# Kernel tuning notes

Hardware: AMD Instinct MI355X
Metric: run time of the kernel (lower is better)

Reference implementation:

```python
import jax, jax.numpy as jnp
import numpy as np

NV, NH = 6000, 6000
DV, DH = 1024, 1024
HID, HEADS = 128, 3
EV, EH, EC = 200000, 200000, 32768


def _gat(x, ei, W, a_src, a_dst, bias, edge_attr=None, lin_e=None, a_e=None):
    """PyG GATConv (heads=H, concat=False, add_self_loops=True, LeakyReLU 0.2).
    Returns (node_out [N,C], alpha [E+N, H])."""
    N = x.shape[0]
    H, C = a_src.shape
    xw = (x @ W).reshape(N, H, C)                      # [N,H,C]
    asrc = jnp.einsum('nhc,hc->nh', xw, a_src)         # [N,H]
    adst = jnp.einsum('nhc,hc->nh', xw, a_dst)
    loop = jnp.arange(N, dtype=ei.dtype)               # self-loops appended
    src = jnp.concatenate([ei[0], loop])
    dst = jnp.concatenate([ei[1], loop])
    alpha = asrc[src] + adst[dst]                      # [E+N,H]
    if edge_attr is not None:
        # edge_dim=1 path: lin_edge(weight)[E,H,C] dotted with att_edge; self-loop attr = mean (PyG fill_value='mean')
        ea = jnp.concatenate([edge_attr, jnp.full((N,), jnp.mean(edge_attr), edge_attr.dtype)])
        ef = (ea[:, None] * lin_e[None, :]).reshape(-1, H, C)
        alpha = alpha + jnp.einsum('ehc,hc->eh', ef, a_e)
    alpha = jax.nn.leaky_relu(alpha, 0.2)
    # segment softmax over incoming edges of each destination node
    amax = jax.ops.segment_max(alpha, dst, num_segments=N)
    ex = jnp.exp(alpha - amax[dst])
    den = jax.ops.segment_sum(ex, dst, num_segments=N)
    alpha = ex / (den[dst] + 1e-16)
    out = jax.ops.segment_sum(xw[src] * alpha[..., None], dst, num_segments=N)
    return out.mean(axis=1) + bias, alpha              # concat=False -> head mean


def _bn(x, g, b):  # BatchNorm1d, training mode (batch stats, biased var)
    m = x.mean(0)
    v = x.var(0)
    return (x - m) / jnp.sqrt(v + 1e-5) * g + b


def reference(virus_data, host_data, coexistence_data, virus_edge_weight, host_edge_weight,
              vW, v_asrc, v_adst, v_bias, v_line, v_atte,
              hW, h_asrc, h_adst, h_bias, h_line, h_atte,
              vhW, vh_asrc, vh_adst, vh_bias,
              hvW, hv_asrc, hv_adst, hv_bias,
              linv_W, linv_b, linh_W, linh_b, bn_g, bn_b,
              virus_edge_index, host_edge_index, coexistence_edge_index, coexistence_edge_index_t):
    feat_v, alpha_v = _gat(virus_data, virus_edge_index, vW, v_asrc, v_adst, v_bias,
                           virus_edge_weight, v_line, v_atte)
    feat_h, alpha_h = _gat(host_data, host_edge_index, hW, h_asrc, h_adst, h_bias,
                           host_edge_weight, h_line, h_atte)
    feat_vh, alpha_vh = _gat(coexistence_data, coexistence_edge_index_t, vhW, vh_asrc, vh_adst, vh_bias)
    feat_hv, alpha_hv = _gat(coexistence_data.T, coexistence_edge_index, hvW, hv_asrc, hv_adst, hv_bias)

    vh = jax.nn.leaky_relu(_bn(virus_data @ linv_W + linv_b, bn_g, bn_b), 0.01)
    hh = jax.nn.leaky_relu(_bn(host_data @ linh_W + linh_b, bn_g, bn_b), 0.01)

    output_host = vh @ hh.T                  # [Nv,Nh]
    output_virus = (hh @ vh.T).T             # [Nv,Nh]
    return (output_host, output_virus, output_host + output_virus,
            alpha_v, alpha_h, alpha_vh, alpha_hv,
            feat_v, feat_h, feat_vh, feat_hv)


def setup_inputs() -> dict:
    key = jax.random.key(0)
    ks = iter(jax.random.split(key, 48))

    def nrm(shape, s=0.05):
        return (jax.random.normal(next(ks), shape, jnp.float32) * s).astype(jnp.float32)

    def gat_params(din, edge=True):
        p = [nrm((din, HEADS * HID)), nrm((HEADS, HID)), nrm((HEADS, HID)), jnp.zeros((HID,), jnp.float32)]
        if edge:
            p += [nrm((HEADS * HID,)), nrm((HEADS, HID))]
        return p

    inp = {
        'virus_data': jax.random.normal(next(ks), (NV, DV), jnp.float32),
        'host_data': jax.random.normal(next(ks), (NH, DH), jnp.float32),
        'coexistence_data': jax.random.normal(next(ks), (DV, DH), jnp.float32),
        'virus_edge_weight': jax.random.uniform(next(ks), (EV,), jnp.float32),
        'host_edge_weight': jax.random.uniform(next(ks), (EH,), jnp.float32),
    }
    for pref, din, edge in [('v', DV, True), ('h', DH, True)]:
        W, asrc, adst, b, le, ae = gat_params(din, True)
        inp.update({f'{pref}W': W, f'{pref}_asrc': asrc, f'{pref}_adst': adst,
                    f'{pref}_bias': b, f'{pref}_line': le, f'{pref}_atte': ae})
    for pref, din in [('vh', DH), ('hv', DV)]:
        W, asrc, adst, b = gat_params(din, False)
        inp.update({f'{pref}W': W, f'{pref}_asrc': asrc, f'{pref}_adst': adst, f'{pref}_bias': b})
    inp.update({
        'linv_W': nrm((DV, HID)), 'linv_b': jnp.zeros((HID,), jnp.float32),
        'linh_W': nrm((DH, HID)), 'linh_b': jnp.zeros((HID,), jnp.float32),
        'bn_g': jnp.ones((HID,), jnp.float32), 'bn_b': jnp.zeros((HID,), jnp.float32),
        'virus_edge_index': jax.random.randint(next(ks), (2, EV), 0, NV, jnp.int32),
        'host_edge_index': jax.random.randint(next(ks), (2, EH), 0, NH, jnp.int32),
        'coexistence_edge_index': jax.random.randint(next(ks), (2, EC), 0, DH, jnp.int32),
        'coexistence_edge_index_t': jax.random.randint(next(ks), (2, EC), 0, DV, jnp.int32),
    })
    return inp
```

## Files before the change

kernel.cpp:

```cpp
#include <hip/hip_runtime.h>

#define NV   6000
#define NH   6000
#define HID  128
#define EV   200000
#define EH   200000
#define EC   32768

typedef __attribute__((ext_vector_type(8))) short bf16x8;
typedef __attribute__((ext_vector_type(4))) float f32x4;

__device__ __forceinline__ unsigned short f2bf(float f){
  unsigned u = __float_as_uint(f);
  u += 0x7FFFu + ((u >> 16) & 1u);
  return (unsigned short)(u >> 16);
}

__global__ __launch_bounds__(256) void k_prep_cv(
    const float* __restrict__ virus, const float* __restrict__ hostd, const float* __restrict__ coex,
    unsigned short* __restrict__ Avb, unsigned short* __restrict__ Ahb, unsigned short* __restrict__ Acb){
  int i = blockIdx.x * 256 + threadIdx.x;
  const float* src; unsigned short* dst; int off;
  if (i < 1536000)      { src = virus; dst = Avb; off = i; }
  else if (i < 3072000) { src = hostd; dst = Ahb; off = i - 1536000; }
  else                  { src = coex;  dst = Acb; off = i - 3072000; }
  float4 v = reinterpret_cast<const float4*>(src)[off];
  ushort4 o; o.x = f2bf(v.x); o.y = f2bf(v.y); o.z = f2bf(v.z); o.w = f2bf(v.w);
  reinterpret_cast<ushort4*>(dst)[off] = o;
}

__global__ __launch_bounds__(256) void k_prep_tp(
    const float* __restrict__ coex, const float* __restrict__ vW, const float* __restrict__ linvW,
    const float* __restrict__ hW, const float* __restrict__ linhW,
    const float* __restrict__ vhW, const float* __restrict__ hvW,
    unsigned short* __restrict__ Actb, unsigned short* __restrict__ BtV,
    unsigned short* __restrict__ BtH, unsigned short* __restrict__ BtVH,
    unsigned short* __restrict__ BtHV){
  int idx = blockIdx.x * 256 + threadIdx.x;
  const float* src; unsigned short* dst; int Nc, off, local;
  if      (idx < 1048576){ src=coex;  dst=Actb; Nc=1024; off=0;   local=idx; }
  else if (idx < 1441792){ src=vW;    dst=BtV;  Nc=384;  off=0;   local=idx-1048576; }
  else if (idx < 1572864){ src=linvW; dst=BtV;  Nc=128;  off=384; local=idx-1441792; }
  else if (idx < 1966080){ src=hW;    dst=BtH;  Nc=384;  off=0;   local=idx-1572864; }
  else if (idx < 2097152){ src=linhW; dst=BtH;  Nc=128;  off=384; local=idx-1966080; }
  else if (idx < 2490368){ src=vhW;   dst=BtVH; Nc=384;  off=0;   local=idx-2097152; }
  else                   { src=hvW;   dst=BtHV; Nc=384;  off=0;   local=idx-2490368; }
  int n = local >> 10, k = local & 1023;
  dst[(size_t)(n + off) * 1024 + k] = f2bf(src[(size_t)k * Nc + n]);
}

template<bool TRIPLE>
__device__ __forceinline__ void gemm_nt_body(
    const unsigned short* __restrict__ A, const unsigned short* __restrict__ B,
    int M, int N, int K, int lda, int ldb,
    float* __restrict__ C0, float* __restrict__ C1o, float* __restrict__ C2o, int ldc,
    int bx, int by)
{
  const int tid  = threadIdx.x;
  const int lane = tid & 63, w = tid >> 6;
  const int wr = w >> 1, wc = w & 1;
  const int R  = by * 128 + wr * 64;
  const int Cb = bx * 128 + wc * 64;
  const int r0 = lane & 15, kg = lane >> 4;

  const unsigned short* pa[4]; const unsigned short* pb[4];
  bool va[4], vb[4];
#pragma unroll
  for (int i = 0; i < 4; i++){
    int row = R + i * 16 + r0;
    va[i] = row < M;
    pa[i] = A + (size_t)(va[i] ? row : 0) * lda + kg * 8;
    int col = Cb + i * 16 + r0;
    vb[i] = col < N;
    pb[i] = B + (size_t)(vb[i] ? col : 0) * ldb + kg * 8;
  }
  const bf16x8 Z8 = {0,0,0,0,0,0,0,0};
  f32x4 acc[4][4];
#pragma unroll
  for (int i = 0; i < 4; i++)
#pragma unroll
    for (int j = 0; j < 4; j++) acc[i][j] = (f32x4){0.f,0.f,0.f,0.f};

  for (int kk = 0; kk < K; kk += 32){
    bf16x8 av[4], bv[4];
#pragma unroll
    for (int i = 0; i < 4; i++){
      bf16x8 ta = *reinterpret_cast<const bf16x8*>(pa[i] + kk);
      bf16x8 tb = *reinterpret_cast<const bf16x8*>(pb[i] + kk);
      av[i] = va[i] ? ta : Z8;
      bv[i] = vb[i] ? tb : Z8;
    }
#pragma unroll
    for (int i = 0; i < 4; i++)
#pragma unroll
      for (int j = 0; j < 4; j++)
        acc[i][j] = __builtin_amdgcn_mfma_f32_16x16x32_bf16(av[i], bv[j], acc[i][j], 0, 0, 0);
  }

  const int cn = lane & 15, rq = (lane >> 4) * 4;
#pragma unroll
  for (int i = 0; i < 4; i++){
    int row0 = R + i * 16 + rq;
#pragma unroll
    for (int j = 0; j < 4; j++){
      int col = Cb + j * 16 + cn;
      if (col < N){
#pragma unroll
        for (int r = 0; r < 4; r++){
          int row = row0 + r;
          if (row < M){
            size_t idx = (size_t)row * ldc + col;
            float v = acc[i][j][r];
            C0[idx] = v;
            if (TRIPLE){ C1o[idx] = v; C2o[idx] = v + v; }
          }
        }
      }
    }
  }
}

__global__ __launch_bounds__(256) void k_gemm4(
    const unsigned short* A0, const unsigned short* B0, float* Co0,
    const unsigned short* A1, const unsigned short* B1, float* Co1,
    const unsigned short* A2, const unsigned short* B2, float* Co2,
    const unsigned short* A3, const unsigned short* B3, float* Co3)
{
  int z = blockIdx.z;
  if (z == 0)
    gemm_nt_body<false>(A0, B0, NV, 512, 1024, 1024, 1024, Co0, nullptr, nullptr, 512, blockIdx.x, blockIdx.y);
  else if (z == 1)
    gemm_nt_body<false>(A1, B1, NH, 512, 1024, 1024, 1024, Co1, nullptr, nullptr, 512, blockIdx.x, blockIdx.y);
  else {
    if (blockIdx.x >= 3 || blockIdx.y >= 8) return;
    if (z == 2)
      gemm_nt_body<false>(A2, B2, 1024, 384, 1024, 1024, 1024, Co2, nullptr, nullptr, 384, blockIdx.x, blockIdx.y);
    else
      gemm_nt_body<false>(A3, B3, 1024, 384, 1024, 1024, 1024, Co3, nullptr, nullptr, 384, blockIdx.x, blockIdx.y);
  }
}

__global__ __launch_bounds__(256) void k_gemm_final(
    const unsigned short* __restrict__ A, const unsigned short* __restrict__ B,
    float* __restrict__ o0, float* __restrict__ o1, float* __restrict__ o2)
{
  gemm_nt_body<true>(A, B, NV, NH, 128, 128, 128, o0, o1, o2, NH, blockIdx.x, blockIdx.y);
}

__global__ __launch_bounds__(128) void k_scal(
    const float* vW, const float* v_as, const float* v_ad,
    const float* hW, const float* h_as, const float* h_ad,
    const float* vhW, const float* vh_as, const float* vh_ad,
    const float* hvW, const float* hv_as, const float* hv_ad,
    float* WasV, float* WadV, float* WasH, float* WadH,
    float* WasC1, float* WadC1, float* WasC2, float* WadC2,
    const float* vew, const float* hew, float* sums,
    const float* v_line, const float* v_atte, const float* h_line, const float* h_atte,
    float* Kbuf)
{
  int b = blockIdx.x, t = threadIdx.x;
  int lane = t & 63, w = t >> 6;
  __shared__ float sh[2][2];
  if (b < 4096){
    const float *W, *as_, *ad_; float *Was, *Wad;
    switch (b >> 10){
      case 0:  W=vW;  as_=v_as;  ad_=v_ad;  Was=WasV;  Wad=WadV;  break;
      case 1:  W=hW;  as_=h_as;  ad_=h_ad;  Was=WasH;  Wad=WadH;  break;
      case 2:  W=vhW; as_=vh_as; ad_=vh_ad; Was=WasC1; Wad=WadC1; break;
      default: W=hvW; as_=hv_as; ad_=hv_ad; Was=WasC2; Wad=WadC2; break;
    }
    int k = b & 1023;
    const float* Wr = W + (size_t)k * 384;
    for (int h = 0; h < 3; h++){
      float x = Wr[h*128 + t];
      float s = x * as_[h*128 + t], d = x * ad_[h*128 + t];
      for (int off = 32; off > 0; off >>= 1){ s += __shfl_down(s, off); d += __shfl_down(d, off); }
      if (lane == 0){ sh[w][0] = s; sh[w][1] = d; }
      __syncthreads();
      if (t == 0){ Was[k*3+h] = sh[0][0] + sh[1][0]; Wad[k*3+h] = sh[0][1] + sh[1][1]; }
      __syncthreads();
    }
  } else if (b < 4352){
    const float* x = (b < 4224) ? vew : hew;
    int slot = (b < 4224) ? 0 : 1;
    int base = (b - 4096) & 127;
    float s = 0.f;
    for (int i = base*128 + t; i < EV; i += 128*128) s += x[i];
    for (int off = 32; off > 0; off >>= 1) s += __shfl_down(s, off);
    if (lane == 0) sh[w][0] = s;
    __syncthreads();
    if (t == 0) atomicAdd(&sums[slot], sh[0][0] + sh[1][0]);
  } else {
    for (int h = 0; h < 3; h++){
      float s = v_line[h*128+t] * v_atte[h*128+t];
      for (int off = 32; off > 0; off >>= 1) s += __shfl_down(s, off);
      if (lane == 0) sh[w][0] = s;
      __syncthreads();
      if (t == 0) Kbuf[h] = sh[0][0] + sh[1][0];
      __syncthreads();
      s = h_line[h*128+t] * h_atte[h*128+t];
      for (int off = 32; off > 0; off >>= 1) s += __shfl_down(s, off);
      if (lane == 0) sh[w][0] = s;
      __syncthreads();
      if (t == 0) Kbuf[3+h] = sh[0][0] + sh[1][0];
      __syncthreads();
    }
  }
}

__global__ __launch_bounds__(256) void k_nodedot(
    const float* __restrict__ virus, const float* __restrict__ hostd, const float* __restrict__ coex,
    const float* __restrict__ WasV, const float* __restrict__ WadV,
    const float* __restrict__ WasH, const float* __restrict__ WadH,
    const float* __restrict__ WasC1, const float* __restrict__ WadC1,
    float* asV, float* adV, float* asH, float* adH, float* asC1, float* adC1)
{
  int b = blockIdx.x, t = threadIdx.x;
  const float *xb, *Was, *Wad; float *ao, *doo;
  if (b < 6000)       { int n=b;        xb=virus+(size_t)n*1024; Was=WasV;  Wad=WadV;  ao=asV+n*3;  doo=adV+n*3; }
  else if (b < 12000) { int n=b-6000;   xb=hostd+(size_t)n*1024; Was=WasH;  Wad=WadH;  ao=asH+n*3;  doo=adH+n*3; }
  else                { int n=b-12000;  xb=coex +(size_t)n*1024; Was=WasC1; Wad=WadC1; ao=asC1+n*3; doo=adC1+n*3; }
  float v[6] = {0,0,0,0,0,0};
  for (int k = t; k < 1024; k += 256){
    float xv = xb[k];
    v[0] += xv * Was[k*3+0]; v[1] += xv * Was[k*3+1]; v[2] += xv * Was[k*3+2];
    v[3] += xv * Wad[k*3+0]; v[4] += xv * Wad[k*3+1]; v[5] += xv * Wad[k*3+2];
  }
  __shared__ float sh[4][6];
  int lane = t & 63, w = t >> 6;
  for (int off = 32; off > 0; off >>= 1)
#pragma unroll
    for (int i = 0; i < 6; i++) v[i] += __shfl_down(v[i], off);
  if (lane == 0)
#pragma unroll
    for (int i = 0; i < 6; i++) sh[w][i] = v[i];
  __syncthreads();
  if (t < 6){
    float r = sh[0][t] + sh[1][t] + sh[2][t] + sh[3][t];
    if (t < 3) ao[t] = r; else doo[t-3] = r;
  }
}

__global__ __launch_bounds__(256) void k_nodedot_t(
    const float* __restrict__ coex, const float* __restrict__ Was, const float* __restrict__ Wad,
    float* __restrict__ as_, float* __restrict__ ad_)
{
  __shared__ float sw[3072], sd[3072];
  for (int i = threadIdx.x; i < 3072; i += 256){ sw[i] = Was[i]; sd[i] = Wad[i]; }
  __syncthreads();
  int nn = blockIdx.x * 256 + threadIdx.x;
  float a0=0,a1=0,a2=0,b0=0,b1=0,b2=0;
  for (int k = 0; k < 1024; k++){
    float xv = coex[(size_t)k*1024 + nn];
    a0 += xv*sw[k*3];   a1 += xv*sw[k*3+1]; a2 += xv*sw[k*3+2];
    b0 += xv*sd[k*3];   b1 += xv*sd[k*3+1]; b2 += xv*sd[k*3+2];
  }
  as_[nn*3]=a0; as_[nn*3+1]=a1; as_[nn*3+2]=a2;
  ad_[nn*3]=b0; ad_[nn*3+1]=b1; ad_[nn*3+2]=b2;
}

__global__ __launch_bounds__(256) void k_hist4(
    const int* vd, const int* hd, const int* c1d, const int* c2d,
    int* cV, int* cH, int* c1, int* c2)
{
  int idx = blockIdx.x * 256 + threadIdx.x;
  if (idx >= EV + EH + 2*EC) return;
  const int* dp; int* cnt; int e;
  if      (idx < EV)          { dp=vd;  cnt=cV; e=idx; }
  else if (idx < EV+EH)       { dp=hd;  cnt=cH; e=idx-EV; }
  else if (idx < EV+EH+EC)    { dp=c1d; cnt=c1; e=idx-EV-EH; }
  else                        { dp=c2d; cnt=c2; e=idx-EV-EH-EC; }
  atomicAdd(&cnt[dp[e]], 1);
}

__global__ __launch_bounds__(256) void k_exscan4(
    int* cV, int* sV, int* cH, int* sH, int* c1, int* s1, int* c2, int* s2)
{
  int* cnt; int* st; int N;
  switch (blockIdx.x){
    case 0:  cnt=cV; st=sV; N=NV;   break;
    case 1:  cnt=cH; st=sH; N=NH;   break;
    case 2:  cnt=c1; st=s1; N=1024; break;
    default: cnt=c2; st=s2; N=1024; break;
  }
  __shared__ int sh[256];
  int t = threadIdx.x;
  int chunk = (N + 255) >> 8;
  int lo = t * chunk, hi = lo + chunk;
  if (hi > N) hi = N;
  if (lo > N) lo = N;
  int s = 0;
  for (int i = lo; i < hi; i++) s += cnt[i];
  sh[t] = s;
  __syncthreads();
  for (int off = 1; off < 256; off <<= 1){
    int v = (t >= off) ? sh[t - off] : 0;
    __syncthreads();
    sh[t] += v;
    __syncthreads();
  }
  int run = sh[t] - s;
  for (int i = lo; i < hi; i++){ st[i] = run; run += cnt[i]; }
  if (t == 255) st[N] = sh[255];
}

__global__ __launch_bounds__(256) void k_scatter4(
    const int* vd, const int* hd, const int* c1d, const int* c2d,
    const int* stV, const int* stH, const int* st1, const int* st2,
    int* cuV, int* cuH, int* cu1, int* cu2,
    int* soV, int* soH, int* so1, int* so2)
{
  int idx = blockIdx.x * 256 + threadIdx.x;
  if (idx >= EV + EH + 2*EC) return;
  const int* dp; const int* st; int* cur; int* so; int e;
  if      (idx < EV)       { dp=vd;  st=stV; cur=cuV; so=soV; e=idx; }
  else if (idx < EV+EH)    { dp=hd;  st=stH; cur=cuH; so=soH; e=idx-EV; }
  else if (idx < EV+EH+EC) { dp=c1d; st=st1; cur=cu1; so=so1; e=idx-EV-EH; }
  else                     { dp=c2d; st=st2; cur=cu2; so=so2; e=idx-EV-EH-EC; }
  int d = dp[e];
  so[st[d] + atomicAdd(&cur[d], 1)] = e;
}

#define GCAP 512
struct GatDesc {
  const float* xw; const int* src; const int* sorted; const int* starts;
  const float* as_; const float* ad_; const float* Kc; const float* ew; const float* sumw;
  const float* bias; float* alpha; float* feat;
  int ld; int E; float invE;
};

__global__ __launch_bounds__(128) void k_gat(GatDesc d){
  const int n = blockIdx.x, t = threadIdx.x;
  const int lane = t & 63, w = t >> 6;
  __shared__ float shx[GCAP][3];
  __shared__ int   shs[GCAP];
  __shared__ float redA[2][3], redB[2][3];
  const int s0 = d.starts[n];
  const int deg = d.starts[n+1] - s0;
  const bool hasW = (d.ew != nullptr);
  float K0=0.f, K1=0.f, K2=0.f, wself=0.f;
  if (hasW){ K0=d.Kc[0]; K1=d.Kc[1]; K2=d.Kc[2]; wself = d.sumw[0] * d.invE; }
  const float ad0 = d.ad_[n*3], ad1 = d.ad_[n*3+1], ad2 = d.ad_[n*3+2];
  float sr0 = d.as_[n*3+0] + ad0 + wself*K0;  sr0 = sr0 >= 0.f ? sr0 : 0.2f*sr0;
  float sr1 = d.as_[n*3+1] + ad1 + wself*K1;  sr1 = sr1 >= 0.f ? sr1 : 0.2f*sr1;
  float sr2 = d.as_[n*3+2] + ad2 + wself*K2;  sr2 = sr2 >= 0.f ? sr2 : 0.2f*sr2;

  float mx0 = sr0, mx1 = sr1, mx2 = sr2;
  for (int i = t; i < deg; i += 128){
    int e = d.sorted[s0 + i];
    int s = d.src[e];
    float wv = hasW ? d.ew[e] : 0.f;
    float r0 = d.as_[s*3+0] + ad0 + wv*K0;  r0 = r0 >= 0.f ? r0 : 0.2f*r0;
    float r1 = d.as_[s*3+1] + ad1 + wv*K1;  r1 = r1 >= 0.f ? r1 : 0.2f*r1;
    float r2 = d.as_[s*3+2] + ad2 + wv*K2;  r2 = r2 >= 0.f ? r2 : 0.2f*r2;
    if (i < GCAP){ shs[i] = s; shx[i][0]=r0; shx[i][1]=r1; shx[i][2]=r2; }
    mx0 = fmaxf(mx0, r0); mx1 = fmaxf(mx1, r1); mx2 = fmaxf(mx2, r2);
  }
  for (int off = 32; off > 0; off >>= 1){
    mx0 = fmaxf(mx0, __shfl_down(mx0, off));
    mx1 = fmaxf(mx1, __shfl_down(mx1, off));
    mx2 = fmaxf(mx2, __shfl_down(mx2, off));
  }
  if (lane == 0){ redA[w][0]=mx0; redA[w][1]=mx1; redA[w][2]=mx2; }
  __syncthreads();
  const float M0 = fmaxf(redA[0][0], redA[1][0]);
  const float M1 = fmaxf(redA[0][1], redA[1][1]);
  const float M2 = fmaxf(redA[0][2], redA[1][2]);

  float t0 = 0.f, t1 = 0.f, t2 = 0.f;
  for (int i = t; i < deg; i += 128){
    float r0, r1, r2;
    if (i < GCAP){ r0 = shx[i][0]; r1 = shx[i][1]; r2 = shx[i][2]; }
    else {
      int e = d.sorted[s0 + i]; int s = d.src[e];
      float wv = hasW ? d.ew[e] : 0.f;
      r0 = d.as_[s*3+0] + ad0 + wv*K0; r0 = r0>=0.f?r0:0.2f*r0;
      r1 = d.as_[s*3+1] + ad1 + wv*K1; r1 = r1>=0.f?r1:0.2f*r1;
      r2 = d.as_[s*3+2] + ad2 + wv*K2; r2 = r2>=0.f?r2:0.2f*r2;
    }
    float e0 = expf(r0 - M0), e1 = expf(r1 - M1), e2 = expf(r2 - M2);
    if (i < GCAP){ shx[i][0]=e0; shx[i][1]=e1; shx[i][2]=e2; }
    t0 += e0; t1 += e1; t2 += e2;
  }
  for (int off = 32; off > 0; off >>= 1){
    t0 += __shfl_down(t0, off); t1 += __shfl_down(t1, off); t2 += __shfl_down(t2, off);
  }
  if (lane == 0){ redB[w][0]=t0; redB[w][1]=t1; redB[w][2]=t2; }
  __syncthreads();
  const float se0 = expf(sr0 - M0), se1 = expf(sr1 - M1), se2 = expf(sr2 - M2);
  const float i0 = 1.f / (redB[0][0] + redB[1][0] + se0 + 1e-16f);
  const float i1 = 1.f / (redB[0][1] + redB[1][1] + se1 + 1e-16f);
  const float i2 = 1.f / (redB[0][2] + redB[1][2] + se2 + 1e-16f);

  for (int i = t; i < deg; i += 128){
    int e = d.sorted[s0 + i];
    float e0, e1, e2;
    if (i < GCAP){ e0 = shx[i][0]; e1 = shx[i][1]; e2 = shx[i][2]; }
    else {
      int s = d.src[e];
      float wv = hasW ? d.ew[e] : 0.f;
      float r0 = d.as_[s*3+0]+ad0+wv*K0; r0=r0>=0.f?r0:0.2f*r0;
      float r1 = d.as_[s*3+1]+ad1+wv*K1; r1=r1>=0.f?r1:0.2f*r1;
      float r2 = d.as_[s*3+2]+ad2+wv*K2; r2=r2>=0.f?r2:0.2f*r2;
      e0 = expf(r0-M0); e1 = expf(r1-M1); e2 = expf(r2-M2);
    }
    float* ap = d.alpha + (size_t)e * 3;
    ap[0] = e0 * i0; ap[1] = e1 * i1; ap[2] = e2 * i2;
  }
  if (t == 0){
    float* ap = d.alpha + (size_t)(d.E + n) * 3;
    ap[0] = se0 * i0; ap[1] = se1 * i1; ap[2] = se2 * i2;
  }

  const float* xn = d.xw + (size_t)n * d.ld;
  float f0 = xn[t] * se0, f1 = xn[128+t] * se1, f2 = xn[256+t] * se2;
  for (int i = 0; i < deg; i++){
    int s; float e0, e1, e2;
    if (i < GCAP){ s = shs[i]; e0 = shx[i][0]; e1 = shx[i][1]; e2 = shx[i][2]; }
    else {
      int e = d.sorted[s0 + i]; s = d.src[e];
      float wv = hasW ? d.ew[e] : 0.f;
      float r0 = d.as_[s*3+0]+ad0+wv*K0; r0=r0>=0.f?r0:0.2f*r0;
      float r1 = d.as_[s*3+1]+ad1+wv*K1; r1=r1>=0.f?r1:0.2f*r1;
      float r2 = d.as_[s*3+2]+ad2+wv*K2; r2=r2>=0.f?r2:0.2f*r2;
      e0 = expf(r0-M0); e1 = expf(r1-M1); e2 = expf(r2-M2);
    }
    const float* xs = d.xw + (size_t)s * d.ld;
    f0 += xs[t] * e0; f1 += xs[128+t] * e1; f2 += xs[256+t] * e2;
  }
  d.feat[(size_t)n*128 + t] = (f0*i0 + f1*i1 + f2*i2) * (1.f/3.f) + d.bias[t];
}

__global__ __launch_bounds__(128) void k_bnstat(
    const float* __restrict__ C1, const float* __restrict__ C2, float* __restrict__ bnacc)
{
  int which = blockIdx.y, t = threadIdx.x;
  const float* C = which ? C2 : C1;
  int r0 = blockIdx.x * 32;
  float s = 0.f, q = 0.f;
  for (int r = 0; r < 32; r++){
    int row = r0 + r;
    if (row < NV){
      float v = C[(size_t)row * 512 + 384 + t];
      s += v; q += v * v;
    }
  }
  atomicAdd(&bnacc[which*256 + t],       s);
  atomicAdd(&bnacc[which*256 + 128 + t], q);
}

__global__ __launch_bounds__(256) void k_bnfin(
    const float* __restrict__ bnacc, float* meanV, float* rstdV, float* meanH, float* rstdH)
{
  int t = threadIdx.x;
  int which = t >> 7, j = t & 127;
  float mu = bnacc[which*256 + j] * (1.f/NV);
  float var = bnacc[which*256 + 128 + j] * (1.f/NV) - mu*mu;
  if (which == 0){ meanV[j] = mu; rstdV[j] = rsqrtf(var + 1e-5f); }
  else           { meanH[j] = mu; rstdH[j] = rsqrtf(var + 1e-5f); }
}

__global__ __launch_bounds__(256) void k_bnapply(
    const float* __restrict__ C1, const float* __restrict__ C2,
    const float* __restrict__ meanV, const float* __restrict__ rstdV,
    const float* __restrict__ meanH, const float* __restrict__ rstdH,
    const float* __restrict__ g, const float* __restrict__ b,
    unsigned short* __restrict__ vhb, unsigned short* __restrict__ hhb)
{
  int idx = blockIdx.x * 256 + threadIdx.x;
  int which = idx >= 768000;
  int local = which ? idx - 768000 : idx;
  int m = local >> 7, j = local & 127;
  const float* C = which ? C2 : C1;
  const float* mean = which ? meanH : meanV;
  const float* rstd = which ? rstdH : rstdV;
  unsigned short* out = which ? hhb : vhb;
  float v = (C[(size_t)m*512 + 384 + j] - mean[j]) * rstd[j] * g[j] + b[j];
  v = v >= 0.f ? v : 0.01f * v;
  out[local] = f2bf(v);
}

extern "C" void kernel_launch(void* const* d_in, const int* in_sizes, int n_in,
                              void* d_out, int out_size, void* d_ws, size_t ws_size,
                              hipStream_t stream)
{
  (void)in_sizes; (void)n_in; (void)out_size; (void)ws_size;
  const float* virus  = (const float*)d_in[0];
  const float* hostd  = (const float*)d_in[1];
  const float* coex   = (const float*)d_in[2];
  const float* vew    = (const float*)d_in[3];
  const float* hew    = (const float*)d_in[4];
  const float* vW     = (const float*)d_in[5];
  const float* v_as   = (const float*)d_in[6];
  const float* v_ad   = (const float*)d_in[7];
  const float* v_bias = (const float*)d_in[8];
  const float* v_line = (const float*)d_in[9];
  const float* v_atte = (const float*)d_in[10];
  const float* hW     = (const float*)d_in[11];
  const float* h_as   = (const float*)d_in[12];
  const float* h_ad   = (const float*)d_in[13];
  const float* h_bias = (const float*)d_in[14];
  const float* h_line = (const float*)d_in[15];
  const float* h_atte = (const float*)d_in[16];
  const float* vhW    = (const float*)d_in[17];
  const float* vh_as  = (const float*)d_in[18];
  const float* vh_ad  = (const float*)d_in[19];
  const float* vh_bias= (const float*)d_in[20];
  const float* hvW    = (const float*)d_in[21];
  const float* hv_as  = (const float*)d_in[22];
  const float* hv_ad  = (const float*)d_in[23];
  const float* hv_bias= (const float*)d_in[24];
  const float* linvW  = (const float*)d_in[25];
  const float* linhW  = (const float*)d_in[27];
  const float* bng    = (const float*)d_in[29];
  const float* bnb    = (const float*)d_in[30];
  const int* vei  = (const int*)d_in[31];
  const int* hei  = (const int*)d_in[32];
  const int* cei  = (const int*)d_in[33];
  const int* ceit = (const int*)d_in[34];

  float* out = (float*)d_out;
  float* o0 = out;
  float* o1 = out + 36000000ll;
  float* o2 = out + 72000000ll;
  float* alpha_v  = out + 108000000ll;
  float* alpha_h  = alpha_v  + 618000;
  float* alpha_vh = alpha_h  + 618000;
  float* alpha_hv = alpha_vh + 101376;
  float* feat_v   = alpha_hv + 101376;
  float* feat_h   = feat_v   + 768000;
  float* feat_vh  = feat_h   + 768000;
  float* feat_hv  = feat_vh  + 131072;

  char* wp = (char*)d_ws;
  auto alloc = [&](size_t b) -> void* { void* p = wp; wp += (b + 255) & ~(size_t)255; return p; };
  float* C1 = (float*)alloc((size_t)NV*512*4);
  float* C2 = (float*)alloc((size_t)NH*512*4);
  float* C3 = (float*)alloc((size_t)1024*384*4);
  float* C4 = (float*)alloc((size_t)1024*384*4);
  unsigned short* Avb  = (unsigned short*)alloc((size_t)NV*1024*2);
  unsigned short* Ahb  = (unsigned short*)alloc((size_t)NH*1024*2);
  unsigned short* Acb  = (unsigned short*)alloc((size_t)1024*1024*2);
  unsigned short* Actb = (unsigned short*)alloc((size_t)1024*1024*2);
  unsigned short* BtV  = (unsigned short*)alloc((size_t)512*1024*2);
  unsigned short* BtH  = (unsigned short*)alloc((size_t)512*1024*2);
  unsigned short* BtVH = (unsigned short*)alloc((size_t)384*1024*2);
  unsigned short* BtHV = (unsigned short*)alloc((size_t)384*1024*2);
  unsigned short* vhb  = (unsigned short*)alloc((size_t)NV*128*2);
  unsigned short* hhb  = (unsigned short*)alloc((size_t)NH*128*2);
  float* asV  = (float*)alloc(NV*3*4);   float* adV  = (float*)alloc(NV*3*4);
  float* asH  = (float*)alloc(NH*3*4);   float* adH  = (float*)alloc(NH*3*4);
  float* asC1 = (float*)alloc(1024*3*4); float* adC1 = (float*)alloc(1024*3*4);
  float* asC2 = (float*)alloc(1024*3*4); float* adC2 = (float*)alloc(1024*3*4);
  float* WasV = (float*)alloc(1024*3*4); float* WadV = (float*)alloc(1024*3*4);
  float* WasH = (float*)alloc(1024*3*4); float* WadH = (float*)alloc(1024*3*4);
  float* WasC1= (float*)alloc(1024*3*4); float* WadC1= (float*)alloc(1024*3*4);
  float* WasC2= (float*)alloc(1024*3*4); float* WadC2= (float*)alloc(1024*3*4);
  int* startsV  = (int*)alloc((NV+1)*4);  int* sortedV  = (int*)alloc((size_t)EV*4);
  int* startsH  = (int*)alloc((NH+1)*4);  int* sortedH  = (int*)alloc((size_t)EH*4);
  int* startsC1 = (int*)alloc(1025*4);    int* sortedC1 = (int*)alloc((size_t)EC*4);
  int* startsC2 = (int*)alloc(1025*4);    int* sortedC2 = (int*)alloc((size_t)EC*4);
  float* meanV = (float*)alloc(512); float* rstdV = (float*)alloc(512);
  float* meanH = (float*)alloc(512); float* rstdH = (float*)alloc(512);
  float* Kbuf  = (float*)alloc(256);
  char* z0 = wp;
  int* cntV  = (int*)alloc(NV*4);   int* curV  = (int*)alloc(NV*4);
  int* cntH  = (int*)alloc(NH*4);   int* curH  = (int*)alloc(NH*4);
  int* cntC1 = (int*)alloc(1024*4); int* curC1 = (int*)alloc(1024*4);
  int* cntC2 = (int*)alloc(1024*4); int* curC2 = (int*)alloc(1024*4);
  float* sums  = (float*)alloc(256);
  float* bnacc = (float*)alloc(2*256*4);
  hipMemsetAsync(z0, 0, (size_t)(wp - z0), stream);

  const int* vsrc = vei,  *vdst = vei  + EV;
  const int* hsrc = hei,  *hdst = hei  + EH;
  const int* c1src= ceit, *c1dst= ceit + EC;
  const int* c2src= cei,  *c2dst= cei  + EC;

  k_prep_cv<<<13024, 256, 0, stream>>>(virus, hostd, coex, Avb, Ahb, Acb);
  k_prep_tp<<<11264, 256, 0, stream>>>(coex, vW, linvW, hW, linhW, vhW, hvW,
                                       Actb, BtV, BtH, BtVH, BtHV);
  k_gemm4<<<dim3(4,47,4), 256, 0, stream>>>(Avb, BtV, C1, Ahb, BtH, C2,
                                            Acb, BtVH, C3, Actb, BtHV, C4);
  k_scal<<<4353, 128, 0, stream>>>(vW, v_as, v_ad, hW, h_as, h_ad,
                                   vhW, vh_as, vh_ad, hvW, hv_as, hv_ad,
                                   WasV, WadV, WasH, WadH, WasC1, WadC1, WasC2, WadC2,
                                   vew, hew, sums, v_line, v_atte, h_line, h_atte, Kbuf);
  k_nodedot<<<13024, 256, 0, stream>>>(virus, hostd, coex,
                                       WasV, WadV, WasH, WadH, WasC1, WadC1,
                                       asV, adV, asH, adH, asC1, adC1);
  k_nodedot_t<<<4, 256, 0, stream>>>(coex, WasC2, WadC2, asC2, adC2);
  k_hist4<<<1819, 256, 0, stream>>>(vdst, hdst, c1dst, c2dst, cntV, cntH, cntC1, cntC2);
  k_exscan4<<<4, 256, 0, stream>>>(cntV, startsV, cntH, startsH, cntC1, startsC1, cntC2, startsC2);
  k_scatter4<<<1819, 256, 0, stream>>>(vdst, hdst, c1dst, c2dst,
                                       startsV, startsH, startsC1, startsC2,
                                       curV, curH, curC1, curC2,
                                       sortedV, sortedH, sortedC1, sortedC2);
  {
    GatDesc dv = { C1, vsrc, sortedV, startsV, asV, adV, Kbuf,   vew, &sums[0], v_bias,
                   alpha_v, feat_v, 512, EV, 1.f/EV };
    GatDesc dh = { C2, hsrc, sortedH, startsH, asH, adH, Kbuf+3, hew, &sums[1], h_bias,
                   alpha_h, feat_h, 512, EH, 1.f/EH };
    GatDesc d1 = { C3, c1src, sortedC1, startsC1, asC1, adC1, nullptr, nullptr, nullptr, vh_bias,
                   alpha_vh, feat_vh, 384, EC, 0.f };
    GatDesc d2 = { C4, c2src, sortedC2, startsC2, asC2, adC2, nullptr, nullptr, nullptr, hv_bias,
                   alpha_hv, feat_hv, 384, EC, 0.f };
    k_gat<<<NV,   128, 0, stream>>>(dv);
    k_gat<<<NH,   128, 0, stream>>>(dh);
    k_gat<<<1024, 128, 0, stream>>>(d1);
    k_gat<<<1024, 128, 0, stream>>>(d2);
  }
  k_bnstat<<<dim3(188,2), 128, 0, stream>>>(C1, C2, bnacc);
  k_bnfin<<<1, 256, 0, stream>>>(bnacc, meanV, rstdV, meanH, rstdH);
  k_bnapply<<<6000, 256, 0, stream>>>(C1, C2, meanV, rstdV, meanH, rstdH, bng, bnb, vhb, hhb);
  k_gemm_final<<<dim3(47,47), 256, 0, stream>>>(vhb, hhb, o0, o1, o2);
}
```

Measured before the change: 957.2 us.

## Fuse prep, scalar, histogram, scan, GEMM and GAT stages into fewer kernels

The launch sequence collapses into five kernels. Prep, weight transpose, attention-weight folding, edge histogram and edge-weight sums now share one launch. Scan and node dots share another, the GEMMs share a launch with the CSR scatter, and the four GAT layers are merged with the BatchNorm statistics. The final GEMM applies BatchNorm and leaky-ReLU on the fly, and GEMM outputs are stored as bf16. The transpose now goes through LDS tiles. Together these cut launch count, intermediate fp32 traffic and the separate BN passes, at the cost of bf16 rounding of the xw features and more complex kernels.

```diff
diff --git a/kernel.cpp b/kernel.cpp
--- a/kernel.cpp
+++ b/kernel.cpp
@@ -2,10 +2,10 @@
 
 #define NV   6000
 #define NH   6000
-#define HID  128
 #define EV   200000
 #define EH   200000
 #define EC   32768
+#define GCAP 256
 
 typedef __attribute__((ext_vector_type(8))) short bf16x8;
 typedef __attribute__((ext_vector_type(4))) float f32x4;
@@ -15,45 +15,232 @@
   u += 0x7FFFu + ((u >> 16) & 1u);
   return (unsigned short)(u >> 16);
 }
-
-__global__ __launch_bounds__(256) void k_prep_cv(
+__device__ __forceinline__ float bf2f(unsigned short h){
+  return __uint_as_float((unsigned)h << 16);
+}
+
+__global__ __launch_bounds__(256) void k_prep(
     const float* __restrict__ virus, const float* __restrict__ hostd, const float* __restrict__ coex,
-    unsigned short* __restrict__ Avb, unsigned short* __restrict__ Ahb, unsigned short* __restrict__ Acb){
-  int i = blockIdx.x * 256 + threadIdx.x;
-  const float* src; unsigned short* dst; int off;
-  if (i < 1536000)      { src = virus; dst = Avb; off = i; }
-  else if (i < 3072000) { src = hostd; dst = Ahb; off = i - 1536000; }
-  else                  { src = coex;  dst = Acb; off = i - 3072000; }
-  float4 v = reinterpret_cast<const float4*>(src)[off];
-  ushort4 o; o.x = f2bf(v.x); o.y = f2bf(v.y); o.z = f2bf(v.z); o.w = f2bf(v.w);
-  reinterpret_cast<ushort4*>(dst)[off] = o;
-}
-
-__global__ __launch_bounds__(256) void k_prep_tp(
-    const float* __restrict__ coex, const float* __restrict__ vW, const float* __restrict__ linvW,
+    const float* __restrict__ vW, const float* __restrict__ linvW,
     const float* __restrict__ hW, const float* __restrict__ linhW,
     const float* __restrict__ vhW, const float* __restrict__ hvW,
-    unsigned short* __restrict__ Actb, unsigned short* __restrict__ BtV,
-    unsigned short* __restrict__ BtH, unsigned short* __restrict__ BtVH,
-    unsigned short* __restrict__ BtHV){
-  int idx = blockIdx.x * 256 + threadIdx.x;
-  const float* src; unsigned short* dst; int Nc, off, local;
-  if      (idx < 1048576){ src=coex;  dst=Actb; Nc=1024; off=0;   local=idx; }
-  else if (idx < 1441792){ src=vW;    dst=BtV;  Nc=384;  off=0;   local=idx-1048576; }
-  else if (idx < 1572864){ src=linvW; dst=BtV;  Nc=128;  off=384; local=idx-1441792; }
-  else if (idx < 1966080){ src=hW;    dst=BtH;  Nc=384;  off=0;   local=idx-1572864; }
-  else if (idx < 2097152){ src=linhW; dst=BtH;  Nc=128;  off=384; local=idx-1966080; }
-  else if (idx < 2490368){ src=vhW;   dst=BtVH; Nc=384;  off=0;   local=idx-2097152; }
-  else                   { src=hvW;   dst=BtHV; Nc=384;  off=0;   local=idx-2490368; }
-  int n = local >> 10, k = local & 1023;
-  dst[(size_t)(n + off) * 1024 + k] = f2bf(src[(size_t)k * Nc + n]);
-}
-
-template<bool TRIPLE>
-__device__ __forceinline__ void gemm_nt_body(
+    const float* __restrict__ v_as, const float* __restrict__ v_ad,
+    const float* __restrict__ h_as, const float* __restrict__ h_ad,
+    const float* __restrict__ vh_as, const float* __restrict__ vh_ad,
+    const float* __restrict__ hv_as, const float* __restrict__ hv_ad,
+    const float* __restrict__ vew, const float* __restrict__ hew,
+    const float* __restrict__ v_line, const float* __restrict__ v_atte,
+    const float* __restrict__ h_line, const float* __restrict__ h_atte,
+    const int* __restrict__ vdst, const int* __restrict__ hdst,
+    const int* __restrict__ c1dst, const int* __restrict__ c2dst,
+    unsigned short* Avb, unsigned short* Ahb, unsigned short* Acb,
+    unsigned short* Actb, unsigned short* BtV, unsigned short* BtH,
+    unsigned short* BtVH, unsigned short* BtHV,
+    float* WasV, float* WadV, float* WasH, float* WadH,
+    float* WasC1, float* WadC1, float* WasC2, float* WadC2,
+    float* sums, float* Kbuf,
+    int* cntV, int* cntH, int* cntC1, int* cntC2)
+{
+  __shared__ float tp_lds[64][65];
+  __shared__ float red4[4][2];
+  int b = blockIdx.x, t = threadIdx.x;
+  int lane = t & 63, w = t >> 6;
+
+  if (b < 13024){
+    int i = b * 256 + t;
+    const float* src; unsigned short* dst; int off;
+    if (i < 1536000)      { src = virus; dst = Avb; off = i; }
+    else if (i < 3072000) { src = hostd; dst = Ahb; off = i - 1536000; }
+    else                  { src = coex;  dst = Acb; off = i - 3072000; }
+    float4 v = reinterpret_cast<const float4*>(src)[off];
+    ushort4 o; o.x = f2bf(v.x); o.y = f2bf(v.y); o.z = f2bf(v.z); o.w = f2bf(v.w);
+    reinterpret_cast<ushort4*>(dst)[off] = o;
+    return;
+  }
+  b -= 13024;
+  if (b < 704){
+    const float* src; unsigned short* dst; int Nc, roff, ntn, rel;
+    if      (b < 256){ src=coex;  dst=Actb; Nc=1024; roff=0;   ntn=16; rel=b; }
+    else if (b < 352){ src=vW;    dst=BtV;  Nc=384;  roff=0;   ntn=6;  rel=b-256; }
+    else if (b < 384){ src=linvW; dst=BtV;  Nc=128;  roff=384; ntn=2;  rel=b-352; }
+    else if (b < 480){ src=hW;    dst=BtH;  Nc=384;  roff=0;   ntn=6;  rel=b-384; }
+    else if (b < 512){ src=linhW; dst=BtH;  Nc=128;  roff=384; ntn=2;  rel=b-480; }
+    else if (b < 608){ src=vhW;   dst=BtVH; Nc=384;  roff=0;   ntn=6;  rel=b-512; }
+    else             { src=hvW;   dst=BtHV; Nc=384;  roff=0;   ntn=6;  rel=b-608; }
+    int tn = rel % ntn, tk = rel / ntn;
+    int k0 = tk * 64, n0 = tn * 64;
+    int tx = t & 63, ty = t >> 6;
+#pragma unroll
+    for (int r = 0; r < 16; r++)
+      tp_lds[ty + r*4][tx] = src[(size_t)(k0 + ty + r*4) * Nc + n0 + tx];
+    __syncthreads();
+#pragma unroll
+    for (int r = 0; r < 16; r++)
+      dst[(size_t)(n0 + ty + r*4 + roff) * 1024 + k0 + tx] = f2bf(tp_lds[tx][ty + r*4]);
+    return;
+  }
+  b -= 704;
+  if (b < 2048){
+    int m = b >> 9;
+    int krow = (b & 511) * 2 + (t >> 7);
+    int c = t & 127;
+    const float *W, *as_, *ad_; float *Was, *Wad;
+    switch (m){
+      case 0:  W=vW;  as_=v_as;  ad_=v_ad;  Was=WasV;  Wad=WadV;  break;
+      case 1:  W=hW;  as_=h_as;  ad_=h_ad;  Was=WasH;  Wad=WadH;  break;
+      case 2:  W=vhW; as_=vh_as; ad_=vh_ad; Was=WasC1; Wad=WadC1; break;
+      default: W=hvW; as_=hv_as; ad_=hv_ad; Was=WasC2; Wad=WadC2; break;
+    }
+    const float* Wr = W + (size_t)krow * 384;
+    for (int h = 0; h < 3; h++){
+      float x = Wr[h*128 + c];
+      float s = x * as_[h*128 + c], d = x * ad_[h*128 + c];
+      for (int off = 32; off > 0; off >>= 1){ s += __shfl_down(s, off); d += __shfl_down(d, off); }
+      if (lane == 0){ red4[w][0] = s; red4[w][1] = d; }
+      __syncthreads();
+      if (t == 0)  { Was[krow*3+h] = red4[0][0] + red4[1][0]; Wad[krow*3+h] = red4[0][1] + red4[1][1]; }
+      if (t == 128){ Was[krow*3+h] = red4[2][0] + red4[3][0]; Wad[krow*3+h] = red4[2][1] + red4[3][1]; }
+      __syncthreads();
+    }
+    return;
+  }
+  b -= 2048;
+  if (b < 1819){
+    int idx = b * 256 + t;
+    if (idx >= EV + EH + 2*EC) return;
+    const int* dp; int* cnt; int e;
+    if      (idx < EV)       { dp=vdst;  cnt=cntV;  e=idx; }
+    else if (idx < EV+EH)    { dp=hdst;  cnt=cntH;  e=idx-EV; }
+    else if (idx < EV+EH+EC) { dp=c1dst; cnt=cntC1; e=idx-EV-EH; }
+    else                     { dp=c2dst; cnt=cntC2; e=idx-EV-EH-EC; }
+    atomicAdd(&cnt[dp[e]], 1);
+    return;
+  }
+  b -= 1819;
+  if (b < 256){
+    int which = b >> 7, base = b & 127;
+    const float* x = which ? hew : vew;
+    float s = 0.f;
+    for (int i = base*256 + t; i < EV; i += 128*256) s += x[i];
+    for (int off = 32; off > 0; off >>= 1) s += __shfl_down(s, off);
+    if (lane == 0) red4[w][0] = s;
+    __syncthreads();
+    if (t == 0) atomicAdd(&sums[which], red4[0][0]+red4[1][0]+red4[2][0]+red4[3][0]);
+    return;
+  }
+  for (int h = 0; h < 3; h++){
+    float s = (t < 128) ? v_line[h*128+t] * v_atte[h*128+t] : 0.f;
+    for (int off = 32; off > 0; off >>= 1) s += __shfl_down(s, off);
+    if (lane == 0) red4[w][0] = s;
+    __syncthreads();
+    if (t == 0) Kbuf[h] = red4[0][0]+red4[1][0]+red4[2][0]+red4[3][0];
+    __syncthreads();
+    s = (t < 128) ? h_line[h*128+t] * h_atte[h*128+t] : 0.f;
+    for (int off = 32; off > 0; off >>= 1) s += __shfl_down(s, off);
+    if (lane == 0) red4[w][0] = s;
+    __syncthreads();
+    if (t == 0) Kbuf[3+h] = red4[0][0]+red4[1][0]+red4[2][0]+red4[3][0];
+    __syncthreads();
+  }
+}
+
+__global__ __launch_bounds__(256) void k_nd(
+    int* cntV, int* startsV, int* cntH, int* startsH,
+    int* cntC1, int* startsC1, int* cntC2, int* startsC2,
+    const float* __restrict__ virus, const float* __restrict__ hostd, const float* __restrict__ coex,
+    const float* __restrict__ WasV, const float* __restrict__ WadV,
+    const float* __restrict__ WasH, const float* __restrict__ WadH,
+    const float* __restrict__ WasC1, const float* __restrict__ WadC1,
+    const float* __restrict__ WasC2, const float* __restrict__ WadC2,
+    float* asV, float* adV, float* asH, float* adH,
+    float* asC1, float* adC1, float* asC2, float* adC2)
+{
+  __shared__ int   ssc[256];
+  __shared__ float sh6[4][6];
+  __shared__ float st[8][32][6];
+  int b = blockIdx.x, t = threadIdx.x;
+
+  if (b < 4){
+    int* cnt; int* st_; int N;
+    switch (b){
+      case 0:  cnt=cntV;  st_=startsV;  N=NV;   break;
+      case 1:  cnt=cntH;  st_=startsH;  N=NH;   break;
+      case 2:  cnt=cntC1; st_=startsC1; N=1024; break;
+      default: cnt=cntC2; st_=startsC2; N=1024; break;
+    }
+    int chunk = (N + 255) >> 8;
+    int lo = t * chunk, hi = lo + chunk;
+    if (hi > N) hi = N;
+    if (lo > N) lo = N;
+    int s = 0;
+    for (int i = lo; i < hi; i++) s += cnt[i];
+    ssc[t] = s;
+    __syncthreads();
+    for (int off = 1; off < 256; off <<= 1){
+      int v = (t >= off) ? ssc[t - off] : 0;
+      __syncthreads();
+      ssc[t] += v;
+      __syncthreads();
+    }
+    int run = ssc[t] - s;
+    for (int i = lo; i < hi; i++){ st_[i] = run; run += cnt[i]; }
+    if (t == 255) st_[N] = ssc[255];
+    return;
+  }
+  b -= 4;
+  if (b < 13024){
+    const float *xb, *Was, *Wad; float *ao, *doo;
+    if (b < 6000)       { xb=virus+(size_t)b*1024;        Was=WasV;  Wad=WadV;  ao=asV+b*3;          doo=adV+b*3; }
+    else if (b < 12000) { int n=b-6000;  xb=hostd+(size_t)n*1024; Was=WasH;  Wad=WadH;  ao=asH+n*3;  doo=adH+n*3; }
+    else                { int n=b-12000; xb=coex +(size_t)n*1024; Was=WasC1; Wad=WadC1; ao=asC1+n*3; doo=adC1+n*3; }
+    float v[6] = {0,0,0,0,0,0};
+    for (int k = t; k < 1024; k += 256){
+      float xv = xb[k];
+      v[0] += xv*Was[k*3+0]; v[1] += xv*Was[k*3+1]; v[2] += xv*Was[k*3+2];
+      v[3] += xv*Wad[k*3+0]; v[4] += xv*Wad[k*3+1]; v[5] += xv*Wad[k*3+2];
+    }
+    int lane = t & 63, w = t >> 6;
+    for (int off = 32; off > 0; off >>= 1)
+#pragma unroll
+      for (int i = 0; i < 6; i++) v[i] += __shfl_down(v[i], off);
+    if (lane == 0)
+#pragma unroll
+      for (int i = 0; i < 6; i++) sh6[w][i] = v[i];
+    __syncthreads();
+    if (t < 6){
+      float r = sh6[0][t] + sh6[1][t] + sh6[2][t] + sh6[3][t];
+      if (t < 3) ao[t] = r; else doo[t-3] = r;
+    }
+    return;
+  }
+  b -= 13024;
+  int c = t & 31, ks = t >> 5;
+  int nn = b * 32 + c;
+  float a[6] = {0,0,0,0,0,0};
+  for (int k = ks*128; k < ks*128 + 128; k++){
+    float xv = coex[(size_t)k*1024 + nn];
+    a[0] += xv*WasC2[k*3+0]; a[1] += xv*WasC2[k*3+1]; a[2] += xv*WasC2[k*3+2];
+    a[3] += xv*WadC2[k*3+0]; a[4] += xv*WadC2[k*3+1]; a[5] += xv*WadC2[k*3+2];
+  }
+#pragma unroll
+  for (int j = 0; j < 6; j++) st[ks][c][j] = a[j];
+  __syncthreads();
+  if (t < 32){
+    float r[6] = {0,0,0,0,0,0};
+#pragma unroll
+    for (int k = 0; k < 8; k++)
+#pragma unroll
+      for (int j = 0; j < 6; j++) r[j] += st[k][t][j];
+    int n2 = b * 32 + t;
+    asC2[n2*3] = r[0]; asC2[n2*3+1] = r[1]; asC2[n2*3+2] = r[2];
+    adC2[n2*3] = r[3]; adC2[n2*3+1] = r[4]; adC2[n2*3+2] = r[5];
+  }
+}
+
+template<int MODE>
+__device__ __forceinline__ void gemm_body(
     const unsigned short* __restrict__ A, const unsigned short* __restrict__ B,
-    int M, int N, int K, int lda, int ldb,
-    float* __restrict__ C0, float* __restrict__ C1o, float* __restrict__ C2o, int ldc,
+    int M, int N, unsigned short* __restrict__ xwb, float* __restrict__ lin,
     int bx, int by)
 {
   const int tid  = threadIdx.x;
@@ -69,10 +256,10 @@
   for (int i = 0; i < 4; i++){
     int row = R + i * 16 + r0;
     va[i] = row < M;
-    pa[i] = A + (size_t)(va[i] ? row : 0) * lda + kg * 8;
+    pa[i] = A + (size_t)(va[i] ? row : 0) * 1024 + kg * 8;
     int col = Cb + i * 16 + r0;
     vb[i] = col < N;
-    pb[i] = B + (size_t)(vb[i] ? col : 0) * ldb + kg * 8;
+    pb[i] = B + (size_t)(vb[i] ? col : 0) * 1024 + kg * 8;
   }
   const bf16x8 Z8 = {0,0,0,0,0,0,0,0};
   f32x4 acc[4][4];
@@ -81,7 +268,7 @@
 #pragma unroll
     for (int j = 0; j < 4; j++) acc[i][j] = (f32x4){0.f,0.f,0.f,0.f};
 
-  for (int kk = 0; kk < K; kk += 32){
+  for (int kk = 0; kk < 1024; kk += 32){
     bf16x8 av[4], bv[4];
 #pragma unroll
     for (int i = 0; i < 4; i++){
@@ -109,10 +296,13 @@
         for (int r = 0; r < 4; r++){
           int row = row0 + r;
           if (row < M){
-            size_t idx = (size_t)row * ldc + col;
             float v = acc[i][j][r];
-            C0[idx] = v;
-            if (TRIPLE){ C1o[idx] = v; C2o[idx] = v + v; }
+            if (MODE == 0){
+              if (col < 384) xwb[(size_t)row * 384 + col] = f2bf(v);
+              else           lin[(size_t)row * 128 + col - 384] = v;
+            } else {
+              xwb[(size_t)row * 384 + col] = f2bf(v);
+            }
           }
         }
       }
@@ -120,222 +310,79 @@
   }
 }
 
-__global__ __launch_bounds__(256) void k_gemm4(
-    const unsigned short* A0, const unsigned short* B0, float* Co0,
-    const unsigned short* A1, const unsigned short* B1, float* Co1,
-    const unsigned short* A2, const unsigned short* B2, float* Co2,
-    const unsigned short* A3, const unsigned short* B3, float* Co3)
-{
-  int z = blockIdx.z;
-  if (z == 0)
-    gemm_nt_body<false>(A0, B0, NV, 512, 1024, 1024, 1024, Co0, nullptr, nullptr, 512, blockIdx.x, blockIdx.y);
-  else if (z == 1)
-    gemm_nt_body<false>(A1, B1, NH, 512, 1024, 1024, 1024, Co1, nullptr, nullptr, 512, blockIdx.x, blockIdx.y);
-  else {
-    if (blockIdx.x >= 3 || blockIdx.y >= 8) return;
-    if (z == 2)
-      gemm_nt_body<false>(A2, B2, 1024, 384, 1024, 1024, 1024, Co2, nullptr, nullptr, 384, blockIdx.x, blockIdx.y);
-    else
-      gemm_nt_body<false>(A3, B3, 1024, 384, 1024, 1024, 1024, Co3, nullptr, nullptr, 384, blockIdx.x, blockIdx.y);
-  }
-}
-
-__global__ __launch_bounds__(256) void k_gemm_final(
-    const unsigned short* __restrict__ A, const unsigned short* __restrict__ B,
-    float* __restrict__ o0, float* __restrict__ o1, float* __restrict__ o2)
-{
-  gemm_nt_body<true>(A, B, NV, NH, 128, 128, 128, o0, o1, o2, NH, blockIdx.x, blockIdx.y);
-}
-
-__global__ __launch_bounds__(128) void k_scal(
-    const float* vW, const float* v_as, const float* v_ad,
-    const float* hW, const float* h_as, const float* h_ad,
-    const float* vhW, const float* vh_as, const float* vh_ad,
-    const float* hvW, const float* hv_as, const float* hv_ad,
-    float* WasV, float* WadV, float* WasH, float* WadH,
-    float* WasC1, float* WadC1, float* WasC2, float* WadC2,
-    const float* vew, const float* hew, float* sums,
-    const float* v_line, const float* v_atte, const float* h_line, const float* h_atte,
-    float* Kbuf)
-{
-  int b = blockIdx.x, t = threadIdx.x;
-  int lane = t & 63, w = t >> 6;
-  __shared__ float sh[2][2];
-  if (b < 4096){
-    const float *W, *as_, *ad_; float *Was, *Wad;
-    switch (b >> 10){
-      case 0:  W=vW;  as_=v_as;  ad_=v_ad;  Was=WasV;  Wad=WadV;  break;
-      case 1:  W=hW;  as_=h_as;  ad_=h_ad;  Was=WasH;  Wad=WadH;  break;
-      case 2:  W=vhW; as_=vh_as; ad_=vh_ad; Was=WasC1; Wad=WadC1; break;
-      default: W=hvW; as_=hv_as; ad_=hv_ad; Was=WasC2; Wad=WadC2; break;
-    }
-    int k = b & 1023;
-    const float* Wr = W + (size_t)k * 384;
-    for (int h = 0; h < 3; h++){
-      float x = Wr[h*128 + t];
-      float s = x * as_[h*128 + t], d = x * ad_[h*128 + t];
-      for (int off = 32; off > 0; off >>= 1){ s += __shfl_down(s, off); d += __shfl_down(d, off); }
-      if (lane == 0){ sh[w][0] = s; sh[w][1] = d; }
-      __syncthreads();
-      if (t == 0){ Was[k*3+h] = sh[0][0] + sh[1][0]; Wad[k*3+h] = sh[0][1] + sh[1][1]; }
-      __syncthreads();
-    }
-  } else if (b < 4352){
-    const float* x = (b < 4224) ? vew : hew;
-    int slot = (b < 4224) ? 0 : 1;
-    int base = (b - 4096) & 127;
-    float s = 0.f;
-    for (int i = base*128 + t; i < EV; i += 128*128) s += x[i];
-    for (int off = 32; off > 0; off >>= 1) s += __shfl_down(s, off);
-    if (lane == 0) sh[w][0] = s;
-    __syncthreads();
-    if (t == 0) atomicAdd(&sums[slot], sh[0][0] + sh[1][0]);
-  } else {
-    for (int h = 0; h < 3; h++){
-      float s = v_line[h*128+t] * v_atte[h*128+t];
-      for (int off = 32; off > 0; off >>= 1) s += __shfl_down(s, off);
-      if (lane == 0) sh[w][0] = s;
-      __syncthreads();
-      if (t == 0) Kbuf[h] = sh[0][0] + sh[1][0];
-      __syncthreads();
-      s = h_line[h*128+t] * h_atte[h*128+t];
-      for (int off = 32; off > 0; off >>= 1) s += __shfl_down(s, off);
-      if (lane == 0) sh[w][0] = s;
-      __syncthreads();
-      if (t == 0) Kbuf[3+h] = sh[0][0] + sh[1][0];
-      __syncthreads();
-    }
-  }
-}
-
-__global__ __launch_bounds__(256) void k_nodedot(
-    const float* __restrict__ virus, const float* __restrict__ hostd, const float* __restrict__ coex,
-    const float* __restrict__ WasV, const float* __restrict__ WadV,
-    const float* __restrict__ WasH, const float* __restrict__ WadH,
-    const float* __restrict__ WasC1, const float* __restrict__ WadC1,
-    float* asV, float* adV, float* asH, float* adH, float* asC1, float* adC1)
-{
-  int b = blockIdx.x, t = threadIdx.x;
-  const float *xb, *Was, *Wad; float *ao, *doo;
-  if (b < 6000)       { int n=b;        xb=virus+(size_t)n*1024; Was=WasV;  Wad=WadV;  ao=asV+n*3;  doo=adV+n*3; }
-  else if (b < 12000) { int n=b-6000;   xb=hostd+(size_t)n*1024; Was=WasH;  Wad=WadH;  ao=asH+n*3;  doo=adH+n*3; }
-  else                { int n=b-12000;  xb=coex +(size_t)n*1024; Was=WasC1; Wad=WadC1; ao=asC1+n*3; doo=adC1+n*3; }
-  float v[6] = {0,0,0,0,0,0};
-  for (int k = t; k < 1024; k += 256){
-    float xv = xb[k];
-    v[0] += xv * Was[k*3+0]; v[1] += xv * Was[k*3+1]; v[2] += xv * Was[k*3+2];
-    v[3] += xv * Wad[k*3+0]; v[4] += xv * Wad[k*3+1]; v[5] += xv * Wad[k*3+2];
-  }
-  __shared__ float sh[4][6];
-  int lane = t & 63, w = t >> 6;
-  for (int off = 32; off > 0; off >>= 1)
-#pragma unroll
-    for (int i = 0; i < 6; i++) v[i] += __shfl_down(v[i], off);
-  if (lane == 0)
-#pragma unroll
-    for (int i = 0; i < 6; i++) sh[w][i] = v[i];
-  __syncthreads();
-  if (t < 6){
-    float r = sh[0][t] + sh[1][t] + sh[2][t] + sh[3][t];
-    if (t < 3) ao[t] = r; else doo[t-3] = r;
-  }
-}
-
-__global__ __launch_bounds__(256) void k_nodedot_t(
-    const float* __restrict__ coex, const float* __restrict__ Was, const float* __restrict__ Wad,
-    float* __restrict__ as_, float* __restrict__ ad_)
-{
-  __shared__ float sw[3072], sd[3072];
-  for (int i = threadIdx.x; i < 3072; i += 256){ sw[i] = Was[i]; sd[i] = Wad[i]; }
-  __syncthreads();
-  int nn = blockIdx.x * 256 + threadIdx.x;
-  float a0=0,a1=0,a2=0,b0=0,b1=0,b2=0;
-  for (int k = 0; k < 1024; k++){
-    float xv = coex[(size_t)k*1024 + nn];
-    a0 += xv*sw[k*3];   a1 += xv*sw[k*3+1]; a2 += xv*sw[k*3+2];
-    b0 += xv*sd[k*3];   b1 += xv*sd[k*3+1]; b2 += xv*sd[k*3+2];
-  }
-  as_[nn*3]=a0; as_[nn*3+1]=a1; as_[nn*3+2]=a2;
-  ad_[nn*3]=b0; ad_[nn*3+1]=b1; ad_[nn*3+2]=b2;
-}
-
-__global__ __launch_bounds__(256) void k_hist4(
-    const int* vd, const int* hd, const int* c1d, const int* c2d,
-    int* cV, int* cH, int* c1, int* c2)
-{
-  int idx = blockIdx.x * 256 + threadIdx.x;
-  if (idx >= EV + EH + 2*EC) return;
-  const int* dp; int* cnt; int e;
-  if      (idx < EV)          { dp=vd;  cnt=cV; e=idx; }
-  else if (idx < EV+EH)       { dp=hd;  cnt=cH; e=idx-EV; }
-  else if (idx < EV+EH+EC)    { dp=c1d; cnt=c1; e=idx-EV-EH; }
-  else                        { dp=c2d; cnt=c2; e=idx-EV-EH-EC; }
-  atomicAdd(&cnt[dp[e]], 1);
-}
-
-__global__ __launch_bounds__(256) void k_exscan4(
-    int* cV, int* sV, int* cH, int* sH, int* c1, int* s1, int* c2, int* s2)
-{
-  int* cnt; int* st; int N;
-  switch (blockIdx.x){
-    case 0:  cnt=cV; st=sV; N=NV;   break;
-    case 1:  cnt=cH; st=sH; N=NH;   break;
-    case 2:  cnt=c1; st=s1; N=1024; break;
-    default: cnt=c2; st=s2; N=1024; break;
-  }
-  __shared__ int sh[256];
-  int t = threadIdx.x;
-  int chunk = (N + 255) >> 8;
-  int lo = t * chunk, hi = lo + chunk;
-  if (hi > N) hi = N;
-  if (lo > N) lo = N;
-  int s = 0;
-  for (int i = lo; i < hi; i++) s += cnt[i];
-  sh[t] = s;
-  __syncthreads();
-  for (int off = 1; off < 256; off <<= 1){
-    int v = (t >= off) ? sh[t - off] : 0;
-    __syncthreads();
-    sh[t] += v;
-    __syncthreads();
-  }
-  int run = sh[t] - s;
-  for (int i = lo; i < hi; i++){ st[i] = run; run += cnt[i]; }
-  if (t == 255) st[N] = sh[255];
-}
-
-__global__ __launch_bounds__(256) void k_scatter4(
-    const int* vd, const int* hd, const int* c1d, const int* c2d,
+__global__ __launch_bounds__(256) void k_sg(
+    const unsigned short* Avb, const unsigned short* BtV, unsigned short* xwbV, float* linV,
+    const unsigned short* Ahb, const unsigned short* BtH, unsigned short* xwbH, float* linH,
+    const unsigned short* Acb,  const unsigned short* BtVH, unsigned short* xwbC1,
+    const unsigned short* Actb, const unsigned short* BtHV, unsigned short* xwbC2,
+    const int* vdst, const int* hdst, const int* c1dst, const int* c2dst,
     const int* stV, const int* stH, const int* st1, const int* st2,
     int* cuV, int* cuH, int* cu1, int* cu2,
     int* soV, int* soH, int* so1, int* so2)
 {
-  int idx = blockIdx.x * 256 + threadIdx.x;
+  int b = blockIdx.x;
+  if (b < 424){
+    if (b < 188)      gemm_body<0>(Avb,  BtV,  NV,   512, xwbV,  linV, b & 3, b >> 2);
+    else if (b < 376){ int g = b - 188; gemm_body<0>(Ahb,  BtH,  NH,   512, xwbH,  linH, g & 3, g >> 2); }
+    else if (b < 400){ int g = b - 376; gemm_body<1>(Acb,  BtVH, 1024, 384, xwbC1, nullptr, g % 3, g / 3); }
+    else             { int g = b - 400; gemm_body<1>(Actb, BtHV, 1024, 384, xwbC2, nullptr, g % 3, g / 3); }
+    return;
+  }
+  int idx = (b - 424) * 256 + threadIdx.x;
   if (idx >= EV + EH + 2*EC) return;
   const int* dp; const int* st; int* cur; int* so; int e;
-  if      (idx < EV)       { dp=vd;  st=stV; cur=cuV; so=soV; e=idx; }
-  else if (idx < EV+EH)    { dp=hd;  st=stH; cur=cuH; so=soH; e=idx-EV; }
-  else if (idx < EV+EH+EC) { dp=c1d; st=st1; cur=cu1; so=so1; e=idx-EV-EH; }
-  else                     { dp=c2d; st=st2; cur=cu2; so=so2; e=idx-EV-EH-EC; }
+  if      (idx < EV)       { dp=vdst;  st=stV; cur=cuV; so=soV; e=idx; }
+  else if (idx < EV+EH)    { dp=hdst;  st=stH; cur=cuH; so=soH; e=idx-EV; }
+  else if (idx < EV+EH+EC) { dp=c1dst; st=st1; cur=cu1; so=so1; e=idx-EV-EH; }
+  else                     { dp=c2dst; st=st2; cur=cu2; so=so2; e=idx-EV-EH-EC; }
   int d = dp[e];
   so[st[d] + atomicAdd(&cur[d], 1)] = e;
 }
 
-#define GCAP 512
 struct GatDesc {
-  const float* xw; const int* src; const int* sorted; const int* starts;
+  const unsigned short* xwb; const int* src; const int* sorted; const int* starts;
   const float* as_; const float* ad_; const float* Kc; const float* ew; const float* sumw;
   const float* bias; float* alpha; float* feat;
-  int ld; int E; float invE;
+  int E; float invE;
 };
 
-__global__ __launch_bounds__(128) void k_gat(GatDesc d){
-  const int n = blockIdx.x, t = threadIdx.x;
+__global__ __launch_bounds__(256) void k_gatbn(
+    GatDesc dV, GatDesc dH, GatDesc d1, GatDesc d2,
+    const float* __restrict__ linV, const float* __restrict__ linH, float* __restrict__ bnacc)
+{
+  int b = blockIdx.x, t = threadIdx.x;
+  if (b >= 14048){
+    int bb = b - 14048;
+    int which = bb >= 188;
+    int r0 = (which ? bb - 188 : bb) * 32 + (t >> 7) * 16;
+    int c = t & 127;
+    const float* lin = which ? linH : linV;
+    float s = 0.f, q = 0.f;
+#pragma unroll
+    for (int r = 0; r < 16; r++){
+      int row = r0 + r;
+      if (row < NV){
+        float v = lin[(size_t)row * 128 + c];
+        s += v; q += v * v;
+      }
+    }
+    atomicAdd(&bnacc[which*256 + c],       s);
+    atomicAdd(&bnacc[which*256 + 128 + c], q);
+    return;
+  }
+  GatDesc d; int n;
+  if (b < 6000)       { d = dV; n = b; }
+  else if (b < 12000) { d = dH; n = b - 6000; }
+  else if (b < 13024) { d = d1; n = b - 12000; }
+  else                { d = d2; n = b - 13024; }
+
   const int lane = t & 63, w = t >> 6;
+  const int c = t & 127, half = t >> 7;
   __shared__ float shx[GCAP][3];
   __shared__ int   shs[GCAP];
-  __shared__ float redA[2][3], redB[2][3];
-  const int s0 = d.starts[n];
+  __shared__ float redm[4][3], reds[4][3], shD[128][3];
+
+  const int s0  = d.starts[n];
   const int deg = d.starts[n+1] - s0;
   const bool hasW = (d.ew != nullptr);
   float K0=0.f, K1=0.f, K2=0.f, wself=0.f;
@@ -346,7 +393,7 @@
   float sr2 = d.as_[n*3+2] + ad2 + wself*K2;  sr2 = sr2 >= 0.f ? sr2 : 0.2f*sr2;
 
   float mx0 = sr0, mx1 = sr1, mx2 = sr2;
-  for (int i = t; i < deg; i += 128){
+  for (int i = t; i < deg; i += 256){
     int e = d.sorted[s0 + i];
     int s = d.src[e];
     float wv = hasW ? d.ew[e] : 0.f;
@@ -361,22 +408,22 @@
     mx1 = fmaxf(mx1, __shfl_down(mx1, off));
     mx2 = fmaxf(mx2, __shfl_down(mx2, off));
   }
-  if (lane == 0){ redA[w][0]=mx0; redA[w][1]=mx1; redA[w][2]=mx2; }
+  if (lane == 0){ redm[w][0]=mx0; redm[w][1]=mx1; redm[w][2]=mx2; }
   __syncthreads();
-  const float M0 = fmaxf(redA[0][0], redA[1][0]);
-  const float M1 = fmaxf(redA[0][1], redA[1][1]);
-  const float M2 = fmaxf(redA[0][2], redA[1][2]);
+  const float M0 = fmaxf(fmaxf(redm[0][0],redm[1][0]), fmaxf(redm[2][0],redm[3][0]));
+  const float M1 = fmaxf(fmaxf(redm[0][1],redm[1][1]), fmaxf(redm[2][1],redm[3][1]));
+  const float M2 = fmaxf(fmaxf(redm[0][2],redm[1][2]), fmaxf(redm[2][2],redm[3][2]));
 
   float t0 = 0.f, t1 = 0.f, t2 = 0.f;
-  for (int i = t; i < deg; i += 128){
+  for (int i = t; i < deg; i += 256){
     float r0, r1, r2;
     if (i < GCAP){ r0 = shx[i][0]; r1 = shx[i][1]; r2 = shx[i][2]; }
     else {
       int e = d.sorted[s0 + i]; int s = d.src[e];
       float wv = hasW ? d.ew[e] : 0.f;
-      r0 = d.as_[s*3+0] + ad0 + wv*K0; r0 = r0>=0.f?r0:0.2f*r0;
-      r1 = d.as_[s*3+1] + ad1 + wv*K1; r1 = r1>=0.f?r1:0.2f*r1;
-      r2 = d.as_[s*3+2] + ad2 + wv*K2; r2 = r2>=0.f?r2:0.2f*r2;
+      r0 = d.as_[s*3+0]+ad0+wv*K0; r0 = r0>=0.f?r0:0.2f*r0;
+      r1 = d.as_[s*3+1]+ad1+wv*K1; r1 = r1>=0.f?r1:0.2f*r1;
+      r2 = d.as_[s*3+2]+ad2+wv*K2; r2 = r2>=0.f?r2:0.2f*r2;
     }
     float e0 = expf(r0 - M0), e1 = expf(r1 - M1), e2 = expf(r2 - M2);
     if (i < GCAP){ shx[i][0]=e0; shx[i][1]=e1; shx[i][2]=e2; }
@@ -385,14 +432,14 @@
   for (int off = 32; off > 0; off >>= 1){
     t0 += __shfl_down(t0, off); t1 += __shfl_down(t1, off); t2 += __shfl_down(t2, off);
   }
-  if (lane == 0){ redB[w][0]=t0; redB[w][1]=t1; redB[w][2]=t2; }
+  if (lane == 0){ reds[w][0]=t0; reds[w][1]=t1; reds[w][2]=t2; }
   __syncthreads();
   const float se0 = expf(sr0 - M0), se1 = expf(sr1 - M1), se2 = expf(sr2 - M2);
-  const float i0 = 1.f / (redB[0][0] + redB[1][0] + se0 + 1e-16f);
-  const float i1 = 1.f / (redB[0][1] + redB[1][1] + se1 + 1e-16f);
-  const float i2 = 1.f / (redB[0][2] + redB[1][2] + se2 + 1e-16f);
-
-  for (int i = t; i < deg; i += 128){
+  const float i0 = 1.f / (reds[0][0]+reds[1][0]+reds[2][0]+reds[3][0] + se0 + 1e-16f);
+  const float i1 = 1.f / (reds[0][1]+reds[1][1]+reds[2][1]+reds[3][1] + se1 + 1e-16f);
+  const float i2 = 1.f / (reds[0][2]+reds[1][2]+reds[2][2]+reds[3][2] + se2 + 1e-16f);
+
+  for (int i = t; i < deg; i += 256){
     int e = d.sorted[s0 + i];
     float e0, e1, e2;
     if (i < GCAP){ e0 = shx[i][0]; e1 = shx[i][1]; e2 = shx[i][2]; }
@@ -412,9 +459,12 @@
     ap[0] = se0 * i0; ap[1] = se1 * i1; ap[2] = se2 * i2;
   }
 
-  const float* xn = d.xw + (size_t)n * d.ld;
-  float f0 = xn[t] * se0, f1 = xn[128+t] * se1, f2 = xn[256+t] * se2;
-  for (int i = 0; i < deg; i++){
+  float f0, f1, f2;
+  if (half == 0){
+    const unsigned short* xn = d.xwb + (size_t)n * 384;
+    f0 = bf2f(xn[c]) * se0; f1 = bf2f(xn[128+c]) * se1; f2 = bf2f(xn[256+c]) * se2;
+  } else { f0 = f1 = f2 = 0.f; }
+  for (int i = half; i < deg; i += 2){
     int s; float e0, e1, e2;
     if (i < GCAP){ s = shs[i]; e0 = shx[i][0]; e1 = shx[i][1]; e2 = shx[i][2]; }
     else {
@@ -425,59 +475,107 @@
       float r2 = d.as_[s*3+2]+ad2+wv*K2; r2=r2>=0.f?r2:0.2f*r2;
       e0 = expf(r0-M0); e1 = expf(r1-M1); e2 = expf(r2-M2);
     }
-    const float* xs = d.xw + (size_t)s * d.ld;
-    f0 += xs[t] * e0; f1 += xs[128+t] * e1; f2 += xs[256+t] * e2;
-  }
-  d.feat[(size_t)n*128 + t] = (f0*i0 + f1*i1 + f2*i2) * (1.f/3.f) + d.bias[t];
-}
-
-__global__ __launch_bounds__(128) void k_bnstat(
-    const float* __restrict__ C1, const float* __restrict__ C2, float* __restrict__ bnacc)
+    const unsigned short* xs = d.xwb + (size_t)s * 384;
+    f0 += bf2f(xs[c]) * e0; f1 += bf2f(xs[128+c]) * e1; f2 += bf2f(xs[256+c]) * e2;
+  }
+  if (half == 1){ shD[c][0] = f0; shD[c][1] = f1; shD[c][2] = f2; }
+  __syncthreads();
+  if (half == 0){
+    f0 += shD[c][0]; f1 += shD[c][1]; f2 += shD[c][2];
+    d.feat[(size_t)n*128 + c] = (f0*i0 + f1*i1 + f2*i2) * (1.f/3.f) + d.bias[c];
+  }
+}
+
+__global__ __launch_bounds__(256) void k_fin(
+    const float* __restrict__ linV, const float* __restrict__ linH,
+    const float* __restrict__ bnacc, const float* __restrict__ g, const float* __restrict__ bb,
+    float* __restrict__ o0, float* __restrict__ o1, float* __restrict__ o2)
 {
-  int which = blockIdx.y, t = threadIdx.x;
-  const float* C = which ? C2 : C1;
-  int r0 = blockIdx.x * 32;
-  float s = 0.f, q = 0.f;
-  for (int r = 0; r < 32; r++){
-    int row = r0 + r;
-    if (row < NV){
-      float v = C[(size_t)row * 512 + 384 + t];
-      s += v; q += v * v;
-    }
-  }
-  atomicAdd(&bnacc[which*256 + t],       s);
-  atomicAdd(&bnacc[which*256 + 128 + t], q);
-}
-
-__global__ __launch_bounds__(256) void k_bnfin(
-    const float* __restrict__ bnacc, float* meanV, float* rstdV, float* meanH, float* rstdH)
-{
-  int t = threadIdx.x;
-  int which = t >> 7, j = t & 127;
-  float mu = bnacc[which*256 + j] * (1.f/NV);
-  float var = bnacc[which*256 + 128 + j] * (1.f/NV) - mu*mu;
-  if (which == 0){ meanV[j] = mu; rstdV[j] = rsqrtf(var + 1e-5f); }
-  else           { meanH[j] = mu; rstdH[j] = rsqrtf(var + 1e-5f); }
-}
-
-__global__ __launch_bounds__(256) void k_bnapply(
-    const float* __restrict__ C1, const float* __restrict__ C2,
-    const float* __restrict__ meanV, const float* __restrict__ rstdV,
-    const float* __restrict__ meanH, const float* __restrict__ rstdH,
-    const float* __restrict__ g, const float* __restrict__ b,
-    unsigned short* __restrict__ vhb, unsigned short* __restrict__ hhb)
-{
-  int idx = blockIdx.x * 256 + threadIdx.x;
-  int which = idx >= 768000;
-  int local = which ? idx - 768000 : idx;
-  int m = local >> 7, j = local & 127;
-  const float* C = which ? C2 : C1;
-  const float* mean = which ? meanH : meanV;
-  const float* rstd = which ? rstdH : rstdV;
-  unsigned short* out = which ? hhb : vhb;
-  float v = (C[(size_t)m*512 + 384 + j] - mean[j]) * rstd[j] * g[j] + b[j];
-  v = v >= 0.f ? v : 0.01f * v;
-  out[local] = f2bf(v);
+  __shared__ float sA[128], hA[128], sB[128], hB[128];
+  const int t = threadIdx.x;
+  if (t < 128){
+    float mu  = bnacc[t] * (1.f/NV);
+    float var = bnacc[128+t] * (1.f/NV) - mu*mu;
+    float rs  = rsqrtf(var + 1e-5f);
+    sA[t] = rs * g[t]; hA[t] = bb[t] - mu * rs * g[t];
+  } else {
+    int j = t - 128;
+    float mu  = bnacc[256+j] * (1.f/NV);
+    float var = bnacc[384+j] * (1.f/NV) - mu*mu;
+    float rs  = rsqrtf(var + 1e-5f);
+    sB[j] = rs * g[j]; hB[j] = bb[j] - mu * rs * g[j];
+  }
+  __syncthreads();
+
+  const int lane = t & 63, w = t >> 6;
+  const int wr = w >> 1, wc = w & 1;
+  const int R  = blockIdx.y * 128 + wr * 64;
+  const int Cb = blockIdx.x * 128 + wc * 64;
+  const int r0 = lane & 15, kg = lane >> 4;
+
+  const float* pa[4]; const float* pb[4];
+  bool va[4], vb[4];
+#pragma unroll
+  for (int i = 0; i < 4; i++){
+    int row = R + i * 16 + r0;
+    va[i] = row < NV;
+    pa[i] = linV + (size_t)(va[i] ? row : 0) * 128 + kg * 8;
+    int col = Cb + i * 16 + r0;
+    vb[i] = col < NH;
+    pb[i] = linH + (size_t)(vb[i] ? col : 0) * 128 + kg * 8;
+  }
+  const bf16x8 Z8 = {0,0,0,0,0,0,0,0};
+  f32x4 acc[4][4];
+#pragma unroll
+  for (int i = 0; i < 4; i++)
+#pragma unroll
+    for (int j = 0; j < 4; j++) acc[i][j] = (f32x4){0.f,0.f,0.f,0.f};
+
+  for (int kk = 0; kk < 128; kk += 32){
+    const int kb = kk + kg * 8;
+    bf16x8 av[4], bv[4];
+#pragma unroll
+    for (int i = 0; i < 4; i++){
+      bf16x8 fa, fb;
+#pragma unroll
+      for (int e = 0; e < 8; e++){
+        float v1 = fmaf(pa[i][kk + e], sA[kb + e], hA[kb + e]);
+        v1 = v1 >= 0.f ? v1 : 0.01f * v1;
+        fa[e] = (short)f2bf(v1);
+        float v2 = fmaf(pb[i][kk + e], sB[kb + e], hB[kb + e]);
+        v2 = v2 >= 0.f ? v2 : 0.01f * v2;
+        fb[e] = (short)f2bf(v2);
+      }
+      av[i] = va[i] ? fa : Z8;
+      bv[i] = vb[i] ? fb : Z8;
+    }
+#pragma unroll
+    for (int i = 0; i < 4; i++)
+#pragma unroll
+      for (int j = 0; j < 4; j++)
+        acc[i][j] = __builtin_amdgcn_mfma_f32_16x16x32_bf16(av[i], bv[j], acc[i][j], 0, 0, 0);
+  }
+
+  const int cn = lane & 15, rq = (lane >> 4) * 4;
+#pragma unroll
+  for (int i = 0; i < 4; i++){
+    int row0 = R + i * 16 + rq;
+#pragma unroll
+    for (int j = 0; j < 4; j++){
+      int col = Cb + j * 16 + cn;
+      if (col < NH){
+#pragma unroll
+        for (int r = 0; r < 4; r++){
+          int row = row0 + r;
+          if (row < NV){
+            size_t idx = (size_t)row * NH + col;
+            float v = acc[i][j][r];
+            o0[idx] = v; o1[idx] = v; o2[idx] = v + v;
+          }
+        }
+      }
+    }
+  }
 }
 
 extern "C" void kernel_launch(void* const* d_in, const int* in_sizes, int n_in,
@@ -534,10 +632,6 @@
 
   char* wp = (char*)d_ws;
   auto alloc = [&](size_t b) -> void* { void* p = wp; wp += (b + 255) & ~(size_t)255; return p; };
-  float* C1 = (float*)alloc((size_t)NV*512*4);
-  float* C2 = (float*)alloc((size_t)NH*512*4);
-  float* C3 = (float*)alloc((size_t)1024*384*4);
-  float* C4 = (float*)alloc((size_t)1024*384*4);
   unsigned short* Avb  = (unsigned short*)alloc((size_t)NV*1024*2);
   unsigned short* Ahb  = (unsigned short*)alloc((size_t)NH*1024*2);
   unsigned short* Acb  = (unsigned short*)alloc((size_t)1024*1024*2);
@@ -546,8 +640,12 @@
   unsigned short* BtH  = (unsigned short*)alloc((size_t)512*1024*2);
   unsigned short* BtVH = (unsigned short*)alloc((size_t)384*1024*2);
   unsigned short* BtHV = (unsigned short*)alloc((size_t)384*1024*2);
-  unsigned short* vhb  = (unsigned short*)alloc((size_t)NV*128*2);
-  unsigned short* hhb  = (unsigned short*)alloc((size_t)NH*128*2);
+  unsigned short* xwbV = (unsigned short*)alloc((size_t)NV*384*2);
+  unsigned short* xwbH = (unsigned short*)alloc((size_t)NH*384*2);
+  unsigned short* xwbC1= (unsigned short*)alloc((size_t)1024*384*2);
+  unsigned short* xwbC2= (unsigned short*)alloc((size_t)1024*384*2);
+  float* linV = (float*)alloc((size_t)NV*128*4);
+  float* linH = (float*)alloc((size_t)NH*128*4);
   float* asV  = (float*)alloc(NV*3*4);   float* adV  = (float*)alloc(NV*3*4);
   float* asH  = (float*)alloc(NH*3*4);   float* adH  = (float*)alloc(NH*3*4);
   float* asC1 = (float*)alloc(1024*3*4); float* adC1 = (float*)alloc(1024*3*4);
@@ -560,8 +658,6 @@
   int* startsH  = (int*)alloc((NH+1)*4);  int* sortedH  = (int*)alloc((size_t)EH*4);
   int* startsC1 = (int*)alloc(1025*4);    int* sortedC1 = (int*)alloc((size_t)EC*4);
   int* startsC2 = (int*)alloc(1025*4);    int* sortedC2 = (int*)alloc((size_t)EC*4);
-  float* meanV = (float*)alloc(512); float* rstdV = (float*)alloc(512);
-  float* meanH = (float*)alloc(512); float* rstdH = (float*)alloc(512);
   float* Kbuf  = (float*)alloc(256);
   char* z0 = wp;
   int* cntV  = (int*)alloc(NV*4);   int* curV  = (int*)alloc(NV*4);
@@ -569,7 +665,7 @@
   int* cntC1 = (int*)alloc(1024*4); int* curC1 = (int*)alloc(1024*4);
   int* cntC2 = (int*)alloc(1024*4); int* curC2 = (int*)alloc(1024*4);
   float* sums  = (float*)alloc(256);
-  float* bnacc = (float*)alloc(2*256*4);
+  float* bnacc = (float*)alloc(512*4);
   hipMemsetAsync(z0, 0, (size_t)(wp - z0), stream);
 
   const int* vsrc = vei,  *vdst = vei  + EV;
@@ -577,41 +673,34 @@
   const int* c1src= ceit, *c1dst= ceit + EC;
   const int* c2src= cei,  *c2dst= cei  + EC;
 
-  k_prep_cv<<<13024, 256, 0, stream>>>(virus, hostd, coex, Avb, Ahb, Acb);
-  k_prep_tp<<<11264, 256, 0, stream>>>(coex, vW, linvW, hW, linhW, vhW, hvW,
-                                       Actb, BtV, BtH, BtVH, BtHV);
-  k_gemm4<<<dim3(4,47,4), 256, 0, stream>>>(Avb, BtV, C1, Ahb, BtH, C2,
-                                            Acb, BtVH, C3, Actb, BtHV, C4);
-  k_scal<<<4353, 128, 0, stream>>>(vW, v_as, v_ad, hW, h_as, h_ad,
-                                   vhW, vh_as, vh_ad, hvW, hv_as, hv_ad,
-                                   WasV, WadV, WasH, WadH, WasC1, WadC1, WasC2, WadC2,
-                                   vew, hew, sums, v_line, v_atte, h_line, h_atte, Kbuf);
-  k_nodedot<<<13024, 256, 0, stream>>>(virus, hostd, coex,
-                                       WasV, WadV, WasH, WadH, WasC1, WadC1,
-                                       asV, adV, asH, adH, asC1, adC1);
-  k_nodedot_t<<<4, 256, 0, stream>>>(coex, WasC2, WadC2, asC2, adC2);
-  k_hist4<<<1819, 256, 0, stream>>>(vdst, hdst, c1dst, c2dst, cntV, cntH, cntC1, cntC2);
-  k_exscan4<<<4, 256, 0, stream>>>(cntV, startsV, cntH, startsH, cntC1, startsC1, cntC2, startsC2);
-  k_scatter4<<<1819, 256, 0, stream>>>(vdst, hdst, c1dst, c2dst,
-                                       startsV, startsH, startsC1, startsC2,
-                                       curV, curH, curC1, curC2,
-                                       sortedV, sortedH, sortedC1, sortedC2);
+  k_prep<<<17852, 256, 0, stream>>>(virus, hostd, coex,
+      vW, linvW, hW, linhW, vhW, hvW,
+      v_as, v_ad, h_as, h_ad, vh_as, vh_ad, hv_as, hv_ad,
+      vew, hew, v_line, v_atte, h_line, h_atte,
+      vdst, hdst, c1dst, c2dst,
+      Avb, Ahb, Acb, Actb, BtV, BtH, BtVH, BtHV,
+      WasV, WadV, WasH, WadH, WasC1, WadC1, WasC2, WadC2,
+      sums, Kbuf, cntV, cntH, cntC1, cntC2);
+  k_nd<<<13060, 256, 0, stream>>>(cntV, startsV, cntH, startsH, cntC1, startsC1, cntC2, startsC2,
+      virus, hostd, coex,
+      WasV, WadV, WasH, WadH, WasC1, WadC1, WasC2, WadC2,
+      asV, adV, asH, adH, asC1, adC1, asC2, adC2);
+  k_sg<<<2243, 256, 0, stream>>>(Avb, BtV, xwbV, linV, Ahb, BtH, xwbH, linH,
+      Acb, BtVH, xwbC1, Actb, BtHV, xwbC2,
+      vdst, hdst, c1dst, c2dst,
+      startsV, startsH, startsC1, startsC2,
+      curV, curH, curC1, curC2,
+      sortedV, sortedH, sortedC1, sortedC2);
   {
-    GatDesc dv = { C1, vsrc, sortedV, startsV, asV, adV, Kbuf,   vew, &sums[0], v_bias,
-                   alpha_v, feat_v, 512, EV, 1.f/EV };
-    GatDesc dh = { C2, hsrc, sortedH, startsH, asH, adH, Kbuf+3, hew, &sums[1], h_bias,
-                   alpha_h, feat_h, 512, EH, 1.f/EH };
-    GatDesc d1 = { C3, c1src, sortedC1, startsC1, asC1, adC1, nullptr, nullptr, nullptr, vh_bias,
-                   alpha_vh, feat_vh, 384, EC, 0.f };
-    GatDesc d2 = { C4, c2src, sortedC2, startsC2, asC2, adC2, nullptr, nullptr, nullptr, hv_bias,
-                   alpha_hv, feat_hv, 384, EC, 0.f };
-    k_gat<<<NV,   128, 0, stream>>>(dv);
-    k_gat<<<NH,   128, 0, stream>>>(dh);
-    k_gat<<<1024, 128, 0, stream>>>(d1);
-    k_gat<<<1024, 128, 0, stream>>>(d2);
-  }
-  k_bnstat<<<dim3(188,2), 128, 0, stream>>>(C1, C2, bnacc);
-  k_bnfin<<<1, 256, 0, stream>>>(bnacc, meanV, rstdV, meanH, rstdH);
-  k_bnapply<<<6000, 256, 0, stream>>>(C1, C2, meanV, rstdV, meanH, rstdH, bng, bnb, vhb, hhb);
-  k_gemm_final<<<dim3(47,47), 256, 0, stream>>>(vhb, hhb, o0, o1, o2);
-}
+    GatDesc dv = { xwbV,  vsrc,  sortedV,  startsV,  asV,  adV,  Kbuf,   vew, &sums[0], v_bias,
+                   alpha_v,  feat_v,  EV, 1.f/EV };
+    GatDesc dh = { xwbH,  hsrc,  sortedH,  startsH,  asH,  adH,  Kbuf+3, hew, &sums[1], h_bias,
+                   alpha_h,  feat_h,  EH, 1.f/EH };
+    GatDesc dc1= { xwbC1, c1src, sortedC1, startsC1, asC1, adC1, nullptr, nullptr, nullptr, vh_bias,
+                   alpha_vh, feat_vh, EC, 0.f };
+    GatDesc dc2= { xwbC2, c2src, sortedC2, startsC2, asC2, adC2, nullptr, nullptr, nullptr, hv_bias,
+                   alpha_hv, feat_hv, EC, 0.f };
+    k_gatbn<<<14424, 256, 0, stream>>>(dv, dh, dc1, dc2, linV, linH, bnacc);
+  }
+  k_fin<<<dim3(47,47), 256, 0, stream>>>(linV, linH, bnacc, bng, bnb, o0, o1, o2);
+}
```

Result: faster. 835.9 us (-12.7%).
